# Kernel tuning notes

Hardware: AMD Instinct MI355X
Metric: run time of the kernel (lower is better)

Reference implementation:

```python
import jax, jax.numpy as jnp
import numpy as np
import math

INPUT_WIDTH = 1024
KEY_WIDTH = 64
VALUE_WIDTH = 64
NUM_HEADS = 16
NUM_GROUPS = 4
HEADS_PER_GROUP = NUM_HEADS // NUM_GROUPS  # w = 4


def setup_inputs() -> dict:
    key = jax.random.key(0)
    k_x, k_q, k_k, k_v, k_p = jax.random.split(key, 5)
    n, s = 2, 2048
    # torch.nn.Linear weights are [out, in]; we store transposed [in, out] for x @ W.
    def lin(k, fan_in, fan_out):
        bound = 1.0 / math.sqrt(fan_in)
        return jax.random.uniform(k, (fan_in, fan_out), minval=-bound, maxval=bound, dtype=jnp.float32)
    return {
        "X": jax.random.normal(k_x, (n, s, INPUT_WIDTH), dtype=jnp.float32),
        "Wq": lin(k_q, INPUT_WIDTH, NUM_HEADS * KEY_WIDTH),
        "Wk": lin(k_k, INPUT_WIDTH, NUM_GROUPS * KEY_WIDTH),
        "Wv": lin(k_v, INPUT_WIDTH, NUM_GROUPS * VALUE_WIDTH),
        "Wpost": lin(k_p, NUM_HEADS * VALUE_WIDTH, INPUT_WIDTH),
    }


def reference(X, Wq, Wk, Wv, Wpost):
    n, s, _ = X.shape
    # Projections (no bias)
    Q = (X @ Wq).reshape(n, s, NUM_GROUPS, HEADS_PER_GROUP, KEY_WIDTH)  # [b,s,g,w,e]
    K = (X @ Wk).reshape(n, s, NUM_GROUPS, KEY_WIDTH)                   # [b,t,g,e]
    V = (X @ Wv).reshape(n, s, NUM_GROUPS, VALUE_WIDTH)                 # [b,t,g,e]
    scale = 1.0 / math.sqrt(KEY_WIDTH)
    # Grouped cross-attention: scores [b,s,t,g,w]
    raw = jnp.einsum('bsgwe,btge->bstgw', Q, K * scale)
    attn = jax.nn.softmax(raw, axis=2)  # softmax over key positions t
    A = jnp.einsum('bstgw,btge->bsgwe', attn, V).reshape(n, s, NUM_HEADS * VALUE_WIDTH)
    P = A @ Wpost
    return X + P
```

## Files before the change

### kernel.cpp

```cpp
#include <hip/hip_runtime.h>
#include <hip/hip_bf16.h>
#include <hip/hip_fp16.h>
#include <math.h>

typedef __attribute__((ext_vector_type(8))) short bfrag8;
typedef __attribute__((ext_vector_type(8))) _Float16 hfrag8;
typedef __attribute__((ext_vector_type(4))) float facc4;
typedef __attribute__((ext_vector_type(16))) float facc16;

#define MFMA16B(a, b, c) __builtin_amdgcn_mfma_f32_16x16x32_bf16((a), (b), (c), 0, 0, 0)
#define MFMA32B(a, b, c) __builtin_amdgcn_mfma_f32_32x32x16_bf16((a), (b), (c), 0, 0, 0)
#define MFMA32H(a, b, c) __builtin_amdgcn_mfma_f32_32x32x16_f16((a), (b), (c), 0, 0, 0)

__device__ __forceinline__ void gload_lds16(const void* g, void* l) {
    __builtin_amdgcn_global_load_lds(
        (const __attribute__((address_space(1))) void*)g,
        (__attribute__((address_space(3))) void*)l, 16, 0, 0);
}

__device__ __forceinline__ unsigned short f2bf(float f) {
    unsigned u = __float_as_uint(f);
    u += 0x7fffu + ((u >> 16) & 1u);
    return (unsigned short)(u >> 16);
}

__device__ __forceinline__ unsigned pk2(float a, float b) {
    auto h = __builtin_amdgcn_cvt_pkrtz(a, b);
    union { decltype(h) h; unsigned u; } c;
    c.h = h;
    return c.u;
}

__device__ __forceinline__ void do_transpose(const float* __restrict__ src,
                                             unsigned short* __restrict__ dst,
                                             int Kdim, int N, int nb, int kb,
                                             float (*tile)[33], int tid) {
    int tx = tid & 31, ty = tid >> 5;
#pragma unroll
    for (int r = ty; r < 32; r += 8)
        tile[r][tx] = src[(size_t)(kb + r) * N + nb + tx];
    __syncthreads();
#pragma unroll
    for (int r = ty; r < 32; r += 8)
        dst[(size_t)(nb + r) * Kdim + kb + tx] = f2bf(tile[tx][r]);
}

__global__ __launch_bounds__(256) void k_prep(
    const float* __restrict__ X, const float* __restrict__ Wq,
    const float* __restrict__ Wk, const float* __restrict__ Wv,
    const float* __restrict__ Wp,
    unsigned short* __restrict__ Xb, unsigned short* __restrict__ Wqkvt,
    unsigned short* __restrict__ Wpt) {
    __shared__ float tile[32][33];
    int blk = blockIdx.x, tid = threadIdx.x;
    if (blk < 4096) {
        int i = (blk * 256 + tid) * 4;
        float4 v = *reinterpret_cast<const float4*>(X + i);
        unsigned short o[4] = {f2bf(v.x), f2bf(v.y), f2bf(v.z), f2bf(v.w)};
        *reinterpret_cast<ulonglong1*>(Xb + i) = *reinterpret_cast<ulonglong1*>(o);
    } else if (blk < 5120) {
        int idx = blk - 4096;
        do_transpose(Wq, Wqkvt, 1024, 1024, (idx & 31) * 32, (idx >> 5) * 32, tile, tid);
    } else if (blk < 5376) {
        int idx = blk - 5120;
        do_transpose(Wk, Wqkvt + 1024 * 1024, 1024, 256, (idx & 7) * 32, (idx >> 3) * 32, tile, tid);
    } else if (blk < 5632) {
        int idx = blk - 5376;
        do_transpose(Wv, Wqkvt + 1280 * 1024, 1024, 256, (idx & 7) * 32, (idx >> 3) * 32, tile, tid);
    } else {
        int idx = blk - 5632;
        do_transpose(Wp, Wpt, 1024, 1024, (idx & 31) * 32, (idx >> 5) * 32, tile, tid);
    }
}

template <int EPI>
__global__ __launch_bounds__(512) void k_gemm_bt(
    const unsigned short* __restrict__ A, const unsigned short* __restrict__ Bt,
    int M, int N, int K,
    unsigned short* __restrict__ Qo, unsigned short* __restrict__ Ko,
    unsigned short* __restrict__ Vto,
    const float* __restrict__ Xres, float* __restrict__ Out) {
    __shared__ char lds[65536];
    const int tid = threadIdx.x;
    const int lane = tid & 63, wid = tid >> 6;
    const int wr = wid >> 2, wc = wid & 3;
    const int l15 = lane & 15, lhi = lane >> 4;
    const int m0 = blockIdx.y * 128, n0 = blockIdx.x * 128;
    const int nk = K >> 6;

    facc4 acc[4][2] = {};

    int segbase = wid * 2;
    int p0 = segbase * 1024 + lane * 16;

    auto STAGE = [&](int buf, int k0) {
#pragma unroll
        for (int i = 0; i < 2; ++i) {
            int p = p0 + i * 1024;
            int row = p >> 7;
            int src = (p & 127) ^ ((row & 7) << 4);
            gload_lds16(A + (size_t)(m0 + row) * K + k0 + (src >> 1),
                        lds + buf * 16384 + (segbase + i) * 1024);
            gload_lds16(Bt + (size_t)(n0 + row) * K + k0 + (src >> 1),
                        lds + 32768 + buf * 16384 + (segbase + i) * 1024);
        }
    };

    STAGE(0, 0);
    __syncthreads();

    for (int t = 0; t < nk; ++t) {
        const int cur = t & 1;
        if (t + 1 < nk) STAGE(cur ^ 1, (t + 1) * 64);
        const char* Ab = lds + cur * 16384;
        const char* Bb = lds + 32768 + cur * 16384;
#pragma unroll
        for (int kc = 0; kc < 2; ++kc) {
            bfrag8 af[4], bfv[2];
#pragma unroll
            for (int mi = 0; mi < 4; ++mi) {
                int row = wr * 64 + mi * 16 + l15;
                int off = (row * 128 + kc * 64 + lhi * 16) ^ ((row & 7) << 4);
                af[mi] = *reinterpret_cast<const bfrag8*>(Ab + off);
            }
#pragma unroll
            for (int ni = 0; ni < 2; ++ni) {
                int row = wc * 32 + ni * 16 + l15;
                int off = (row * 128 + kc * 64 + lhi * 16) ^ ((row & 7) << 4);
                bfv[ni] = *reinterpret_cast<const bfrag8*>(Bb + off);
            }
#pragma unroll
            for (int mi = 0; mi < 4; ++mi)
#pragma unroll
                for (int ni = 0; ni < 2; ++ni)
                    acc[mi][ni] = MFMA16B(af[mi], bfv[ni], acc[mi][ni]);
        }
        __syncthreads();
    }

    if (EPI == 0 && n0 >= 1280) {
        unsigned short* VT = (unsigned short*)lds;
#pragma unroll
        for (int mi = 0; mi < 4; ++mi)
#pragma unroll
            for (int ni = 0; ni < 2; ++ni) {
                int col = wc * 32 + ni * 16 + l15;
                int row0 = wr * 64 + mi * 16 + lhi * 4;
                unsigned long long u = 0;
#pragma unroll
                for (int r = 0; r < 4; ++r)
                    u |= (unsigned long long)__half_as_ushort(__float2half(acc[mi][ni][r]))
                         << (16 * r);
                *reinterpret_cast<unsigned long long*>(VT + col * 136 + row0) = u;
            }
        __syncthreads();
        int c = tid >> 2, q4 = tid & 3;
        int b = m0 >> 11;
        int g = ((n0 - 1280) >> 6) + (c >> 6);
        int e = c & 63;
        unsigned short* dstp = Vto + ((size_t)(b * 4 + g) * 64 + e) * 2048 + (m0 & 2047) + q4 * 32;
        const unsigned short* srcp = VT + c * 136 + q4 * 32;
#pragma unroll
        for (int j = 0; j < 4; ++j)
            *(reinterpret_cast<uint4*>(dstp) + j) = *(reinterpret_cast<const uint4*>(srcp) + j);
        return;
    }

#pragma unroll
    for (int mi = 0; mi < 4; ++mi)
#pragma unroll
        for (int ni = 0; ni < 2; ++ni)
#pragma unroll
            for (int r = 0; r < 4; ++r) {
                int grow = m0 + wr * 64 + mi * 16 + lhi * 4 + r;
                int gcol = n0 + wc * 32 + ni * 16 + l15;
                float v = acc[mi][ni][r];
                if (EPI == 0) {
                    int b = grow >> 11, t = grow & 2047;
                    if (gcol < 1024) {
                        Qo[(size_t)grow * 1024 + gcol] = f2bf(v * 0.18033688f);
                    } else {
                        int cc = gcol - 1024;
                        int g = cc >> 6, e = cc & 63;
                        Ko[(((size_t)(b * 4 + g) * 2048 + t) << 6) + e] = f2bf(v);
                    }
                } else {
                    size_t idx = (size_t)grow * 1024 + gcol;
                    Out[idx] = Xres[idx] + v;
                }
            }
}

__global__ __launch_bounds__(512, 4) void k_attn(
    const unsigned short* __restrict__ Q,
    const unsigned short* __restrict__ Kb,
    const unsigned short* __restrict__ Vt,
    unsigned short* __restrict__ Abuf) {
    __shared__ char smem[65536];

    const int tid = threadIdx.x;
    const int lane = tid & 63, wid = tid >> 6;
    const int kvh = wid >> 2, qw = wid & 3;
    const int l31 = lane & 31, hi = lane >> 5;

    int wg = blockIdx.x;
    int swz = ((wg & 7) << 6) | (wg >> 3);
    const int qt = swz & 15, head = (swz >> 4) & 15, b = swz >> 8;
    const int g = head >> 2;
    const size_t kvK = (size_t)(b * 4 + g) * 2048 * 64;
    const size_t kvV = (size_t)(b * 4 + g) * 64 * 2048;
    const int qrow0 = b * 2048 + qt * 128 + qw * 32;

    bfrag8 qf[4];
#pragma unroll
    for (int ks = 0; ks < 4; ++ks)
        qf[ks] = *reinterpret_cast<const bfrag8*>(
            Q + (size_t)(qrow0 + l31) * 1024 + head * 64 + ks * 16 + hi * 8);

    const unsigned short* src[4];
    int ldsoff[4];
#pragma unroll
    for (int j = 0; j < 4; ++j) {
        int seg = (qw << 1) + (j & 1);
        bool isV = j >= 2;
        int p = seg * 1024 + lane * 16;
        int row = p >> 7;
        int sb = (p & 127) ^ ((row & 7) << 4);
        src[j] = !isV ? Kb + kvK + (size_t)(kvh * 64 + row) * 64 + (sb >> 1)
                      : Vt + kvV + (size_t)row * 2048 + kvh * 64 + (sb >> 1);
        ldsoff[j] = (isV ? 32768 : 0) + kvh * 16384 + seg * 1024;
    }

    facc16 o[2] = {};
    float psA = 0.f, psB = 0.f;

#pragma unroll
    for (int j = 0; j < 4; ++j) gload_lds16(src[j], smem + ldsoff[j]);
    __syncthreads();

    for (int t = 0; t < 16; ++t) {
        const int cur = t & 1;
        if (t < 15) {
#pragma unroll
            for (int j = 0; j < 4; ++j)
                gload_lds16(src[j] + (size_t)(t + 1) * (j < 2 ? 128 * 64 : 128),
                            smem + ldsoff[j] + (cur ^ 1) * 8192);
        }
        const char* Kc = smem + kvh * 16384 + cur * 8192;
        const char* Vc = smem + 32768 + kvh * 16384 + cur * 8192;

        facc16 s[2] = {};
        __builtin_amdgcn_s_setprio(1);
#pragma unroll
        for (int ks = 0; ks < 4; ++ks)
#pragma unroll
            for (int nt = 0; nt < 2; ++nt) {
                int row = nt * 32 + l31;
                int off = (row * 128 + ks * 32 + hi * 16) ^ ((row & 7) << 4);
                bfrag8 kf = *reinterpret_cast<const bfrag8*>(Kc + off);
                s[nt] = MFMA32B(kf, qf[ks], s[nt]);
            }
        __builtin_amdgcn_s_setprio(0);

#pragma unroll
        for (int nt = 0; nt < 2; ++nt) {
#pragma unroll
            for (int e = 0; e < 16; e += 2) {
                float e0 = __builtin_amdgcn_exp2f(s[nt][e]);
                float e1 = __builtin_amdgcn_exp2f(s[nt][e + 1]);
                s[nt][e] = e0;
                s[nt][e + 1] = e1;
                psA += e0;
                psB += e1;
            }
#pragma unroll
            for (int kh = 0; kh < 2; ++kh) {
                const int ks = nt * 2 + kh;
                const int pb = kh * 2;
                unsigned a0 = pk2(s[nt][4 * pb + 0], s[nt][4 * pb + 1]);
                unsigned a1 = pk2(s[nt][4 * pb + 2], s[nt][4 * pb + 3]);
                unsigned b0 = pk2(s[nt][4 * pb + 4], s[nt][4 * pb + 5]);
                unsigned b1 = pk2(s[nt][4 * pb + 6], s[nt][4 * pb + 7]);
                asm("v_permlane32_swap_b32 %0, %1" : "+v"(a0), "+v"(b0));
                asm("v_permlane32_swap_b32 %0, %1" : "+v"(a1), "+v"(b1));
                union { unsigned u[4]; hfrag8 h; } pu;
                pu.u[0] = a0; pu.u[1] = a1; pu.u[2] = b0; pu.u[3] = b1;
                __builtin_amdgcn_s_setprio(1);
#pragma unroll
                for (int ot = 0; ot < 2; ++ot) {
                    int row = ot * 32 + l31;
                    int off = (row * 128 + ks * 32 + hi * 16) ^ ((row & 7) << 4);
                    hfrag8 vf = *reinterpret_cast<const hfrag8*>(Vc + off);
                    o[ot] = MFMA32H(vf, pu.h, o[ot]);
                }
                __builtin_amdgcn_s_setprio(0);
            }
        }
        __syncthreads();
    }

    float psum = psA + psB;
    float* cmO = (float*)smem;
    float* cmL = (float*)(smem + 32768);
    if (kvh == 1) {
#pragma unroll
        for (int ot = 0; ot < 2; ++ot)
#pragma unroll
            for (int r = 0; r < 16; ++r)
                cmO[qw * 2048 + (ot * 16 + r) * 64 + lane] = o[ot][r];
        cmL[qw * 64 + lane] = psum;
    }
    __syncthreads();
    if (kvh == 0) {
#pragma unroll
        for (int ot = 0; ot < 2; ++ot)
#pragma unroll
            for (int r = 0; r < 16; ++r)
                o[ot][r] += cmO[qw * 2048 + (ot * 16 + r) * 64 + lane];
        psum += cmL[qw * 64 + lane];

        float l = psum + __shfl_xor(psum, 32, 64);
        float rl = 1.0f / l;
        int arow = qrow0 + l31;
#pragma unroll
        for (int ot = 0; ot < 2; ++ot)
#pragma unroll
            for (int p = 0; p < 4; ++p) {
                unsigned long long u = 0;
#pragma unroll
                for (int r = 0; r < 4; ++r)
                    u |= (unsigned long long)f2bf(o[ot][4 * p + r] * rl) << (16 * r);
                *reinterpret_cast<unsigned long long*>(
                    Abuf + (size_t)arow * 1024 + head * 64 + ot * 32 + p * 8 + hi * 4) = u;
            }
    }
}


extern "C" void kernel_launch(void* const* d_in, const int* in_sizes, int n_in,
                              void* d_out, int out_size, void* d_ws, size_t ws_size,
                              hipStream_t stream) {
    const float* X = (const float*)d_in[0];
    const float* Wq = (const float*)d_in[1];
    const float* Wk = (const float*)d_in[2];
    const float* Wv = (const float*)d_in[3];
    const float* Wpost = (const float*)d_in[4];
    float* Out = (float*)d_out;

    unsigned short* Xb = (unsigned short*)d_ws;
    unsigned short* Wqkvt = Xb + 4096 * 1024;
    unsigned short* Wpt = Wqkvt + 1536 * 1024;
    unsigned short* Qb = Wpt + 1024 * 1024;
    unsigned short* Kbuf = Qb + 4096 * 1024;
    unsigned short* Vtbuf = Kbuf + 8 * 2048 * 64;
    unsigned short* Abuf = Vtbuf + 8 * 2048 * 64;

    k_prep<<<6656, 256, 0, stream>>>(X, Wq, Wk, Wv, Wpost, Xb, Wqkvt, Wpt);

    k_gemm_bt<0><<<dim3(12, 32), 512, 0, stream>>>(Xb, Wqkvt, 4096, 1536, 1024,
                                                   Qb, Kbuf, Vtbuf, nullptr, nullptr);

    k_attn<<<512, 512, 0, stream>>>(Qb, Kbuf, Vtbuf, Abuf);

    k_gemm_bt<1><<<dim3(8, 32), 512, 0, stream>>>(Abuf, Wpt, 4096, 1024, 1024,
                                                  nullptr, nullptr, nullptr, X, Out);
}
```

Measured before the change: 92.29 us.

## Switch attention KV loop to 32-key tiles with triple-buffered async LDS loads

The attention kernel's KV streaming changes from 64-key tiles with double buffering and a full __syncthreads per step to 32-key tiles with a three-slot ring. Each step waits on an explicit vmcnt(2) and a single s_barrier, so the next tile's global-to-LDS load can stay in flight while the current tile is computed. Each KV half-group now walks a contiguous 1024-key range, and the V tile uses a new 64-byte-row swizzle. LDS shrinks from 64KB to 48KB and the occupancy hint drops from 4 to 2 blocks. The cost is twice as many loop iterations, each doing less MFMA work to hide barrier and wait latency.

```diff
diff --git a/kernel.cpp b/kernel.cpp
--- a/kernel.cpp
+++ b/kernel.cpp
@@ -191,12 +191,12 @@
             }
 }
 
-__global__ __launch_bounds__(512, 4) void k_attn(
+__global__ __launch_bounds__(512, 2) void k_attn(
     const unsigned short* __restrict__ Q,
     const unsigned short* __restrict__ Kb,
     const unsigned short* __restrict__ Vt,
     unsigned short* __restrict__ Abuf) {
-    __shared__ char smem[65536];
+    __shared__ char smem[49152];
 
     const int tid = threadIdx.x;
     const int lane = tid & 63, wid = tid >> 6;
@@ -217,87 +217,79 @@
         qf[ks] = *reinterpret_cast<const bfrag8*>(
             Q + (size_t)(qrow0 + l31) * 1024 + head * 64 + ks * 16 + hi * 8);
 
-    const unsigned short* src[4];
-    int ldsoff[4];
-#pragma unroll
-    for (int j = 0; j < 4; ++j) {
-        int seg = (qw << 1) + (j & 1);
-        bool isV = j >= 2;
-        int p = seg * 1024 + lane * 16;
-        int row = p >> 7;
-        int sb = (p & 127) ^ ((row & 7) << 4);
-        src[j] = !isV ? Kb + kvK + (size_t)(kvh * 64 + row) * 64 + (sb >> 1)
-                      : Vt + kvV + (size_t)row * 2048 + kvh * 64 + (sb >> 1);
-        ldsoff[j] = (isV ? 32768 : 0) + kvh * 16384 + seg * 1024;
-    }
+    const int p = qw * 1024 + lane * 16;
+    const int rK = p >> 7;
+    const int cK = (p & 127) ^ ((rK & 7) << 4);
+    const unsigned short* srcK = Kb + kvK + (size_t)(kvh * 1024 + rK) * 64 + (cK >> 1);
+    const int rV = p >> 6;
+    const int cV = (p & 63) ^ ((rV & 6) << 3);
+    const unsigned short* srcV = Vt + kvV + (size_t)rV * 2048 + kvh * 1024 + (cV >> 1);
+    const int dK = kvh * 12288 + qw * 1024;
+    const int dV = 24576 + kvh * 12288 + qw * 1024;
 
     facc16 o[2] = {};
     float psA = 0.f, psB = 0.f;
 
-#pragma unroll
-    for (int j = 0; j < 4; ++j) gload_lds16(src[j], smem + ldsoff[j]);
+    gload_lds16(srcK, smem + dK);
+    gload_lds16(srcV, smem + dV);
+    gload_lds16(srcK + 32 * 64, smem + dK + 4096);
+    gload_lds16(srcV + 32, smem + dV + 4096);
+
+    for (int t = 0; t < 32; ++t) {
+        if (t < 31) asm volatile("s_waitcnt vmcnt(2)" ::: "memory");
+        else        asm volatile("s_waitcnt vmcnt(0)" ::: "memory");
+        __builtin_amdgcn_s_barrier();
+        __builtin_amdgcn_sched_barrier(0);
+        if (t < 30) {
+            const int bn = (t + 2) % 3;
+            gload_lds16(srcK + (size_t)(t + 2) * (32 * 64), smem + dK + bn * 4096);
+            gload_lds16(srcV + (size_t)(t + 2) * 32, smem + dV + bn * 4096);
+        }
+        const char* Kc = smem + kvh * 12288 + (t % 3) * 4096;
+        const char* Vc = smem + 24576 + kvh * 12288 + (t % 3) * 4096;
+
+        facc16 s = {};
+        __builtin_amdgcn_s_setprio(1);
+#pragma unroll
+        for (int ks = 0; ks < 4; ++ks) {
+            int off = (l31 * 128 + ks * 32 + hi * 16) ^ ((l31 & 7) << 4);
+            bfrag8 kf = *reinterpret_cast<const bfrag8*>(Kc + off);
+            s = MFMA32B(kf, qf[ks], s);
+        }
+        __builtin_amdgcn_s_setprio(0);
+
+#pragma unroll
+        for (int e = 0; e < 16; e += 2) {
+            float e0 = __builtin_amdgcn_exp2f(s[e]);
+            float e1 = __builtin_amdgcn_exp2f(s[e + 1]);
+            s[e] = e0;
+            s[e + 1] = e1;
+            psA += e0;
+            psB += e1;
+        }
+#pragma unroll
+        for (int kh = 0; kh < 2; ++kh) {
+            const int pb = kh * 2;
+            unsigned a0 = pk2(s[4 * pb + 0], s[4 * pb + 1]);
+            unsigned a1 = pk2(s[4 * pb + 2], s[4 * pb + 3]);
+            unsigned b0 = pk2(s[4 * pb + 4], s[4 * pb + 5]);
+            unsigned b1 = pk2(s[4 * pb + 6], s[4 * pb + 7]);
+            asm("v_permlane32_swap_b32 %0, %1" : "+v"(a0), "+v"(b0));
+            asm("v_permlane32_swap_b32 %0, %1" : "+v"(a1), "+v"(b1));
+            union { unsigned u[4]; hfrag8 h; } pu;
+            pu.u[0] = a0; pu.u[1] = a1; pu.u[2] = b0; pu.u[3] = b1;
+            __builtin_amdgcn_s_setprio(1);
+#pragma unroll
+            for (int ot = 0; ot < 2; ++ot) {
+                int row = ot * 32 + l31;
+                int off = row * 64 + ((kh * 32 + hi * 16) ^ ((row & 6) << 3));
+                hfrag8 vf = *reinterpret_cast<const hfrag8*>(Vc + off);
+                o[ot] = MFMA32H(vf, pu.h, o[ot]);
+            }
+            __builtin_amdgcn_s_setprio(0);
+        }
+    }
     __syncthreads();
-
-    for (int t = 0; t < 16; ++t) {
-        const int cur = t & 1;
-        if (t < 15) {
-#pragma unroll
-            for (int j = 0; j < 4; ++j)
-                gload_lds16(src[j] + (size_t)(t + 1) * (j < 2 ? 128 * 64 : 128),
-                            smem + ldsoff[j] + (cur ^ 1) * 8192);
-        }
-        const char* Kc = smem + kvh * 16384 + cur * 8192;
-        const char* Vc = smem + 32768 + kvh * 16384 + cur * 8192;
-
-        facc16 s[2] = {};
-        __builtin_amdgcn_s_setprio(1);
-#pragma unroll
-        for (int ks = 0; ks < 4; ++ks)
-#pragma unroll
-            for (int nt = 0; nt < 2; ++nt) {
-                int row = nt * 32 + l31;
-                int off = (row * 128 + ks * 32 + hi * 16) ^ ((row & 7) << 4);
-                bfrag8 kf = *reinterpret_cast<const bfrag8*>(Kc + off);
-                s[nt] = MFMA32B(kf, qf[ks], s[nt]);
-            }
-        __builtin_amdgcn_s_setprio(0);
-
-#pragma unroll
-        for (int nt = 0; nt < 2; ++nt) {
-#pragma unroll
-            for (int e = 0; e < 16; e += 2) {
-                float e0 = __builtin_amdgcn_exp2f(s[nt][e]);
-                float e1 = __builtin_amdgcn_exp2f(s[nt][e + 1]);
-                s[nt][e] = e0;
-                s[nt][e + 1] = e1;
-                psA += e0;
-                psB += e1;
-            }
-#pragma unroll
-            for (int kh = 0; kh < 2; ++kh) {
-                const int ks = nt * 2 + kh;
-                const int pb = kh * 2;
-                unsigned a0 = pk2(s[nt][4 * pb + 0], s[nt][4 * pb + 1]);
-                unsigned a1 = pk2(s[nt][4 * pb + 2], s[nt][4 * pb + 3]);
-                unsigned b0 = pk2(s[nt][4 * pb + 4], s[nt][4 * pb + 5]);
-                unsigned b1 = pk2(s[nt][4 * pb + 6], s[nt][4 * pb + 7]);
-                asm("v_permlane32_swap_b32 %0, %1" : "+v"(a0), "+v"(b0));
-                asm("v_permlane32_swap_b32 %0, %1" : "+v"(a1), "+v"(b1));
-                union { unsigned u[4]; hfrag8 h; } pu;
-                pu.u[0] = a0; pu.u[1] = a1; pu.u[2] = b0; pu.u[3] = b1;
-                __builtin_amdgcn_s_setprio(1);
-#pragma unroll
-                for (int ot = 0; ot < 2; ++ot) {
-                    int row = ot * 32 + l31;
-                    int off = (row * 128 + ks * 32 + hi * 16) ^ ((row & 7) << 4);
-                    hfrag8 vf = *reinterpret_cast<const hfrag8*>(Vc + off);
-                    o[ot] = MFMA32H(vf, pu.h, o[ot]);
-                }
-                __builtin_amdgcn_s_setprio(0);
-            }
-        }
-        __syncthreads();
-    }
 
     float psum = psA + psB;
     float* cmO = (float*)smem;
@@ -325,13 +317,13 @@
 #pragma unroll
         for (int ot = 0; ot < 2; ++ot)
 #pragma unroll
-            for (int p = 0; p < 4; ++p) {
+            for (int p2 = 0; p2 < 4; ++p2) {
                 unsigned long long u = 0;
 #pragma unroll
                 for (int r = 0; r < 4; ++r)
-                    u |= (unsigned long long)f2bf(o[ot][4 * p + r] * rl) << (16 * r);
+                    u |= (unsigned long long)f2bf(o[ot][4 * p2 + r] * rl) << (16 * r);
                 *reinterpret_cast<unsigned long long*>(
-                    Abuf + (size_t)arow * 1024 + head * 64 + ot * 32 + p * 8 + hi * 4) = u;
+                    Abuf + (size_t)arow * 1024 + head * 64 + ot * 32 + p2 * 8 + hi * 4) = u;
             }
     }
 }
```

Measured after the change: 92.59 us. Within noise of the previous version (+0.3%).
